# Kernel optimization log

Measured on AMD Instinct MI355X. Metric: run time of the kernel, lower is better.

The kernel has to match this reference:

```python
import jax, jax.numpy as jnp
from jax import lax
import numpy as np

SHAPE = (50, 60, 65)   # -> after net: (17, 27, 32), flatten = 14688
NEG = 0.01             # LeakyReLU default slope
B, N = 8, 80000        # batch size, total active voxels


def _lrelu(x):
    return jnp.where(x >= 0, x, NEG * x)


def _sparse_conv(x, w, b, m):
    # Regular (non-submanifold) sparse conv == dense VALID conv on densified
    # input (inactive sites are 0 so they contribute nothing). Output site is
    # active iff any input site in the kernel footprint is active; bias is
    # added only at active output sites.
    k = w.shape[2]
    y = lax.conv_general_dilated(x, w, (1, 1, 1), 'VALID',
                                 dimension_numbers=('NCDHW', 'OIDHW', 'NCDHW'))
    m2 = lax.reduce_window(m, 0.0, lax.max, (1, 1, k, k, k), (1, 1, 1, 1, 1), 'VALID')
    y = jnp.where(m2 > 0, y + b[None, :, None, None, None], 0.0)
    return y, m2


def _sparse_maxpool(x, m, k):
    # spconv SparseMaxPool: max over ACTIVE sites only (inactive excluded, not 0)
    xm = jnp.where(m > 0, x, -jnp.inf)
    p = lax.reduce_window(xm, -jnp.inf, lax.max, (1, 1, k, k, k), (1, 1, 1, 1, 1), 'VALID')
    m2 = lax.reduce_window(m, 0.0, lax.max, (1, 1, k, k, k), (1, 1, 1, 1, 1), 'VALID')
    return jnp.where(m2 > 0, p, 0.0), m2


def setup_inputs() -> dict:
    key = jax.random.key(0)
    ks = jax.random.split(key, 24)
    D, H, W = SHAPE
    features = jax.random.normal(ks[0], (N, 1), dtype=jnp.float32)
    bi = jax.random.randint(ks[1], (N,), 0, B)
    zi = jax.random.randint(ks[2], (N,), 0, D)
    yi = jax.random.randint(ks[3], (N,), 0, H)
    xi = jax.random.randint(ks[4], (N,), 0, W)
    coors = jnp.stack([bi, zi, yi, xi], axis=1).astype(jnp.int32)
    s = 0.05
    p = {}
    p['w1'] = jax.random.normal(ks[5], (32, 1, 4, 4, 4), jnp.float32) * s
    p['b1'] = jax.random.normal(ks[6], (32,), jnp.float32) * s
    p['w2'] = jax.random.normal(ks[7], (32, 32, 4, 4, 4), jnp.float32) * s
    p['b2'] = jax.random.normal(ks[8], (32,), jnp.float32) * s
    p['w3'] = jax.random.normal(ks[9], (32, 32, 4, 4, 4), jnp.float32) * s
    p['b3'] = jax.random.normal(ks[10], (32,), jnp.float32) * s
    p['w4'] = jax.random.normal(ks[11], (32, 32, 4, 4, 4), jnp.float32) * s
    p['b4'] = jax.random.normal(ks[12], (32,), jnp.float32) * s
    p['w5'] = jax.random.normal(ks[13], (32, 32, 4, 4, 4), jnp.float32) * s
    p['b5'] = jax.random.normal(ks[14], (32,), jnp.float32) * s
    p['w6'] = jax.random.normal(ks[15], (32, 32, 4, 4, 4), jnp.float32) * s
    p['b6'] = jax.random.normal(ks[16], (32,), jnp.float32) * s
    p['w7'] = jax.random.normal(ks[17], (1, 32, 4, 4, 4), jnp.float32) * s
    p['b7'] = jax.random.normal(ks[18], (1,), jnp.float32) * s
    p['W8'] = jax.random.normal(ks[19], (14688, 1000), jnp.float32) * 0.01
    p['b8'] = jax.random.normal(ks[20], (1000,), jnp.float32) * s
    p['W9'] = jax.random.normal(ks[21], (1000, 1000), jnp.float32) * 0.03
    p['b9'] = jax.random.normal(ks[22], (1000,), jnp.float32) * s
    p['W10'] = jax.random.normal(ks[23], (1000, 1), jnp.float32) * 0.03
    p['b10'] = jnp.zeros((1,), jnp.float32)
    return dict(features=features, coors=coors, batch_size=B, **p)


def reference(features, coors, batch_size,
              w1, b1, w2, b2, w3, b3, w4, b4, w5, b5, w6, b6, w7, b7,
              W8, b8, W9, b9, W10, b10):
    D, H, W = SHAPE
    bi, zi, yi, xi = coors[:, 0], coors[:, 1], coors[:, 2], coors[:, 3]
    dense = jnp.zeros((batch_size, 1, D, H, W), features.dtype)
    dense = dense.at[bi, 0, zi, yi, xi].set(features[:, 0])
    mask = jnp.zeros((batch_size, 1, D, H, W), features.dtype)
    mask = mask.at[bi, 0, zi, yi, xi].set(1.0)

    x, m = _sparse_conv(dense, w1, b1, mask); x = _lrelu(x)
    x, m = _sparse_conv(x, w2, b2, m);        x = _lrelu(x)
    x, m = _sparse_maxpool(x, m, 5)
    x, m = _sparse_conv(x, w3, b3, m);        x = _lrelu(x)
    x, m = _sparse_conv(x, w4, b4, m);        x = _lrelu(x)
    x, m = _sparse_maxpool(x, m, 5)
    x, m = _sparse_conv(x, w5, b5, m);        x = _lrelu(x)
    x, m = _sparse_conv(x, w6, b6, m);        x = _lrelu(x)
    x, m = _sparse_conv(x, w7, b7, m);        x = _lrelu(x)
    x, m = _sparse_maxpool(x, m, 5)

    # ToDense (inactive sites already 0) + Flatten -> [B, 14688]
    h = x.reshape(x.shape[0], -1)
    h = _lrelu(h @ W8 + b8)
    h = _lrelu(h @ W9 + b9)
    out = _lrelu(h @ W10 + b10)
    return out
```

## Files before the change

kernel.cpp:

```cpp
#include <hip/hip_runtime.h>
#include <cstddef>


#define NEGSLOPE 0.01f
#define NINF (-3.0e38f)

#define TZ 4
#define TY 4
#define TXT 16
#define IZ 7
#define IY 7
#define IX 19
#define NV (IZ*IY*IX)

typedef __attribute__((ext_vector_type(8)))  short    short8;
typedef __attribute__((ext_vector_type(4)))  unsigned uint4v;
typedef __attribute__((ext_vector_type(16))) float    floatx16;

__device__ __forceinline__ float lrelu(float v) { return v >= 0.f ? v : NEGSLOPE * v; }

__device__ __forceinline__ unsigned short f2bf(float f) {
  unsigned b = __float_as_uint(f);
  return (unsigned short)((b + 0x7fffu + ((b >> 16) & 1u)) >> 16);
}
__device__ __forceinline__ float bf2f(unsigned short h) {
  return __uint_as_float(((unsigned)h) << 16);
}
__device__ __forceinline__ unsigned splitpair(float a, float b, unsigned& lo) {
  unsigned short ha = f2bf(a), hb = f2bf(b);
  unsigned short la = f2bf(a - bf2f(ha)), lb = f2bf(b - bf2f(hb));
  lo = (unsigned)la | ((unsigned)lb << 16);
  return (unsigned)ha | ((unsigned)hb << 16);
}

__device__ __forceinline__ short8 ld_frag(const uint2* s2, int v, int oct) {
  uint2 u0 = s2[v * 5 + oct * 2];
  uint2 u1 = s2[v * 5 + oct * 2 + 1];
  uint4v t; t.x = u0.x; t.y = u0.y; t.z = u1.x; t.w = u1.y;
  return __builtin_bit_cast(short8, t);
}

__global__ void k_claim(const int* __restrict__ coors, unsigned* __restrict__ claim, int N) {
  int i = blockIdx.x * blockDim.x + threadIdx.x;
  if (i >= N) return;
  int b = coors[4*i], z = coors[4*i+1], y = coors[4*i+2], x = coors[4*i+3];
  int v = ((b*50 + z)*60 + y)*65 + x;
  atomicMax(&claim[v], (unsigned)(i + 1));
}

__global__ void k_scatter(const int* __restrict__ coors, const float* __restrict__ feat,
                          const unsigned* __restrict__ claim,
                          float* __restrict__ x0, float* __restrict__ m0, int N) {
  int i = blockIdx.x * blockDim.x + threadIdx.x;
  if (i >= N) return;
  int b = coors[4*i], z = coors[4*i+1], y = coors[4*i+2], x = coors[4*i+3];
  int v = ((b*50 + z)*60 + y)*65 + x;
  m0[v] = 1.f;
  if (claim[v] == (unsigned)(i + 1)) x0[v] = feat[i];
}

__global__ void k_repack(const float* __restrict__ w, float* __restrict__ wr, int CI, int CO) {
  int i = blockIdx.x * blockDim.x + threadIdx.x;
  int tot = CO * CI * 64;
  if (i >= tot) return;
  int k = i & 63;
  int ci = (i >> 6) % CI;
  int co = i / (64 * CI);
  wr[(k * CI + ci) * CO + co] = w[i];
}

__global__ void k_repack_mfma(const float* __restrict__ w, unsigned short* __restrict__ tbl) {
  int i = blockIdx.x * blockDim.x + threadIdx.x;
  if (i >= 64*4*2*64) return;
  int lane = i & 63; int t = i >> 6;
  int pack = t & 1; t >>= 1;
  int pass = t & 3; int tap = t >> 2;
  int co = lane & 31; int oct = lane >> 5;
#pragma unroll
  for (int j = 0; j < 8; ++j) {
    int k = oct * 8 + j;
    int ci = pass * 8 + (k & 7);
    int part = ((k >> 3) ^ pack) & 1;
    float wv = w[((co * 32 + ci) << 6) + tap];
    unsigned short wh = f2bf(wv);
    unsigned short r = part ? f2bf(wv - bf2f(wh)) : wh;
    tbl[(size_t)i * 8 + j] = r;
  }
}

__global__ void kd_z(const float* __restrict__ in, float* __restrict__ o,
                     int Zi, int Yi, int Xi, int Zo, int K, int nI) {
  int gid = blockIdx.x * blockDim.x + threadIdx.x;
  int perOut = Zo * Yi * Xi;
  if (gid >= nI * perOut) return;
  int item = gid / perOut;
  int r = gid - item * perOut;
  int x = r % Xi; int t = r / Xi;
  int y = t % Yi; int z = t / Yi;
  const float* ib = in + (size_t)item * Zi * Yi * Xi;
  float mx = 0.f;
  for (int d = 0; d < K; d++) mx = fmaxf(mx, ib[((z + d) * Yi + y) * Xi + x]);
  o[gid] = mx;
}

__global__ void kd_y(const float* __restrict__ in, float* __restrict__ o,
                     int Zo, int Yi, int Xi, int Yo, int K, int nI) {
  int gid = blockIdx.x * blockDim.x + threadIdx.x;
  int perOut = Zo * Yo * Xi;
  if (gid >= nI * perOut) return;
  int item = gid / perOut;
  int r = gid - item * perOut;
  int x = r % Xi; int t = r / Xi;
  int y = t % Yo; int z = t / Yo;
  const float* ib = in + (size_t)item * Zo * Yi * Xi;
  float mx = 0.f;
  for (int d = 0; d < K; d++) mx = fmaxf(mx, ib[(z * Yi + y + d) * Xi + x]);
  o[gid] = mx;
}

__global__ void kd_x(const float* __restrict__ in, float* __restrict__ o,
                     int Zo, int Yo, int Xi, int Xo, int K, int nI) {
  int gid = blockIdx.x * blockDim.x + threadIdx.x;
  int perOut = Zo * Yo * Xo;
  if (gid >= nI * perOut) return;
  int item = gid / perOut;
  int r = gid - item * perOut;
  int x = r % Xo; int t = r / Xo;
  int y = t % Yo; int z = t / Yo;
  const float* ib = in + (size_t)item * Zo * Yo * Xi;
  float mx = 0.f;
  for (int d = 0; d < K; d++) mx = fmaxf(mx, ib[(z * Yo + y) * Xi + x + d]);
  o[gid] = mx;
}

__global__ __launch_bounds__(256, 4)
void k_conv32m(const float* __restrict__ in, const unsigned short* __restrict__ tbl,
               const float* __restrict__ bias, const float* __restrict__ mo,
               float* __restrict__ out,
               int Zi, int Yi, int Xi, int Zo, int Yo, int Xo,
               int tilesZ, int tilesY, int tilesX) {
  __shared__ unsigned sU[NV * 10];
  const int perIn = Zi * Yi * Xi;
  const int perOut = Zo * Yo * Xo;
  int bid = blockIdx.x;
  int txi = bid % tilesX; bid /= tilesX;
  int tyi = bid % tilesY; bid /= tilesY;
  int tzi = bid % tilesZ; int item = bid / tilesZ;
  const int z0 = tzi * TZ, y0 = tyi * TY, x0 = txi * TXT;
  const int tid = threadIdx.x;
  const int lane = tid & 63;
  const int col = lane & 31;
  const int oct = lane >> 5;
  const int wv  = tid >> 6;

  int lvBase0, lvBase1;
  {
    int vt0 = (2*wv + 0)*32 + col;
    int vt1 = (2*wv + 1)*32 + col;
    lvBase0 = ((vt0 >> 6)*IY + ((vt0 >> 4) & 3))*IX + (vt0 & 15);
    lvBase1 = ((vt1 >> 6)*IY + ((vt1 >> 4) & 3))*IX + (vt1 & 15);
  }

  floatx16 acc0, acc1;
#pragma unroll
  for (int r = 0; r < 16; ++r) { acc0[r] = 0.f; acc1[r] = 0.f; }

  const float* inb = in + (size_t)item * perIn * 32;
  const char* tb = (const char*)tbl + lane * 16;
  uint2* s2 = (uint2*)sU;

#pragma unroll 1
  for (int p = 0; p < 4; ++p) {
    __syncthreads();
    for (int idx = tid; idx < NV; idx += 256) {
      int iz = idx / (IY * IX); int r = idx - iz * (IY * IX);
      int iy = r / IX; int ix = r - iy * IX;
      int gz = z0 + iz, gy = y0 + iy, gx = x0 + ix;
      float4 f0 = make_float4(0.f,0.f,0.f,0.f), f1 = make_float4(0.f,0.f,0.f,0.f);
      if (gz < Zi && gy < Yi && gx < Xi) {
        const float* vp = inb + (size_t)((gz * Yi + gy) * Xi + gx) * 32 + p * 8;
        f0 = *(const float4*)vp;
        f1 = *(const float4*)(vp + 4);
      }
      unsigned l0, l1, l2, l3;
      unsigned h0 = splitpair(f0.x, f0.y, l0);
      unsigned h1 = splitpair(f0.z, f0.w, l1);
      unsigned h2 = splitpair(f1.x, f1.y, l2);
      unsigned h3 = splitpair(f1.z, f1.w, l3);
      s2[idx * 5 + 0] = make_uint2(h0, h1);
      s2[idx * 5 + 1] = make_uint2(h2, h3);
      s2[idx * 5 + 2] = make_uint2(l0, l1);
      s2[idx * 5 + 3] = make_uint2(l2, l3);
    }
    __syncthreads();

    const char* tp = tb + (size_t)p * 2048;
#pragma unroll 2
    for (int tap = 0; tap < 64; ++tap) {
      int kz = tap >> 4, ky = (tap >> 2) & 3, kx = tap & 3;
      int sOff = (kz * IY + ky) * IX + kx;
      short8 b0 = *(const short8*)(tp + (size_t)tap * 8192);
      short8 b1 = *(const short8*)(tp + (size_t)tap * 8192 + 1024);
      short8 a0 = ld_frag(s2, lvBase0 + sOff, oct);
      short8 a1 = ld_frag(s2, lvBase1 + sOff, oct);
      acc0 = __builtin_amdgcn_mfma_f32_32x32x16_bf16(a0, b0, acc0, 0, 0, 0);
      acc0 = __builtin_amdgcn_mfma_f32_32x32x16_bf16(a0, b1, acc0, 0, 0, 0);
      acc1 = __builtin_amdgcn_mfma_f32_32x32x16_bf16(a1, b0, acc1, 0, 0, 0);
      acc1 = __builtin_amdgcn_mfma_f32_32x32x16_bf16(a1, b1, acc1, 0, 0, 0);
    }
  }

  const float bco = bias[col];
#pragma unroll
  for (int gg = 0; gg < 2; ++gg) {
    int vtb = (2*wv + gg) * 32;
#pragma unroll
    for (int rg = 0; rg < 16; ++rg) {
      int row = (rg & 3) + 8 * (rg >> 2) + 4 * oct;
      int vt = vtb + row;
      int oz = vt >> 6, oy = (vt >> 4) & 3, ox = vt & 15;
      int gz = z0 + oz, gy = y0 + oy, gx = x0 + ox;
      if (gz < Zo && gy < Yo && gx < Xo) {
        int ov = item * perOut + (gz * Yo + gy) * Xo + gx;
        float val = (gg == 0) ? acc0[rg] : acc1[rg];
        bool act = mo[ov] > 0.f;
        out[(size_t)ov * 32 + col] = lrelu(act ? (val + bco) : 0.f);
      }
    }
  }
}

__global__ __launch_bounds__(256, 2)
void k_conv1t(const float* __restrict__ in, const float* __restrict__ wr,
              const float* __restrict__ bias, const float* __restrict__ mo,
              float* __restrict__ out,
              int Zi, int Yi, int Xi, int Zo, int Yo, int Xo,
              int tilesZ, int tilesY, int tilesX) {
  __shared__ float sinf[NV];
  __shared__ float4 wsh[512];
  {
    const float4* wr4 = (const float4*)wr;
    for (int idx = threadIdx.x; idx < 512; idx += 256) wsh[idx] = wr4[idx];
  }
  const int perIn = Zi * Yi * Xi;
  const int perOut = Zo * Yo * Xo;
  int bid = blockIdx.x;
  int txi = bid % tilesX; bid /= tilesX;
  int tyi = bid % tilesY; bid /= tilesY;
  int tzi = bid % tilesZ; int item = bid / tilesZ;
  const int z0 = tzi * TZ, y0 = tyi * TY, x0 = txi * TXT;
  const int tid = threadIdx.x;
  const int ox = tid & 15, oy = (tid >> 4) & 3, oz = tid >> 6;

  const float* inb = in + (size_t)item * perIn;
  for (int idx = tid; idx < NV; idx += 256) {
    int iz = idx / (IY * IX); int r = idx - iz * (IY * IX);
    int iy = r / IX; int ix = r - iy * IX;
    int gz = z0 + iz, gy = y0 + iy, gx = x0 + ix;
    float val = 0.f;
    if (gz < Zi && gy < Yi && gx < Xi)
      val = inb[(size_t)((gz * Yi + gy) * Xi + gx)];
    sinf[idx] = val;
  }
  __syncthreads();

  float4 acc[8];
#pragma unroll
  for (int j = 0; j < 8; ++j) acc[j] = make_float4(0.f, 0.f, 0.f, 0.f);

#pragma unroll 1
  for (int tap = 0; tap < 64; ++tap) {
    int kz = tap >> 4, ky = (tap >> 2) & 3, kx = tap & 3;
    int lv = ((oz + kz) * IY + (oy + ky)) * IX + (ox + kx);
    float av = sinf[lv];
#pragma unroll
    for (int j = 0; j < 8; ++j) {
      float4 wvv = wsh[tap * 8 + j];
      acc[j].x = fmaf(av, wvv.x, acc[j].x);
      acc[j].y = fmaf(av, wvv.y, acc[j].y);
      acc[j].z = fmaf(av, wvv.z, acc[j].z);
      acc[j].w = fmaf(av, wvv.w, acc[j].w);
    }
  }

  int gz = z0 + oz, gy = y0 + oy, gx = x0 + ox;
  if (gz < Zo && gy < Yo && gx < Xo) {
    int ov = item * perOut + (gz * Yo + gy) * Xo + gx;
    bool act = mo[ov] > 0.f;
    const float4* b4 = (const float4*)bias;
    float* op = out + (size_t)ov * 32;
#pragma unroll
    for (int j = 0; j < 8; ++j) {
      float4 r = acc[j]; float4 bj = b4[j];
      r.x = lrelu(act ? (r.x + bj.x) : 0.f);
      r.y = lrelu(act ? (r.y + bj.y) : 0.f);
      r.z = lrelu(act ? (r.z + bj.z) : 0.f);
      r.w = lrelu(act ? (r.w + bj.w) : 0.f);
      *(float4*)(op + j * 4) = r;
    }
  }
}

__global__ __launch_bounds__(256, 2)
void k_conv7t(const float* __restrict__ in, const float* __restrict__ wr,
              const float* __restrict__ bias, const float* __restrict__ mo,
              float* __restrict__ out,
              int Zi, int Yi, int Xi, int Zo, int Yo, int Xo,
              int tilesZ, int tilesY, int tilesX) {
  __shared__ float4 sin4[4][NV];
  __shared__ float4 wsh[512];
  {
    const float4* wr4 = (const float4*)wr;
    for (int idx = threadIdx.x; idx < 512; idx += 256) wsh[idx] = wr4[idx];
  }
  const int perIn = Zi * Yi * Xi;
  const int perOut = Zo * Yo * Xo;
  int bid = blockIdx.x;
  int txi = bid % tilesX; bid /= tilesX;
  int tyi = bid % tilesY; bid /= tilesY;
  int tzi = bid % tilesZ; int item = bid / tilesZ;
  const int z0 = tzi * TZ, y0 = tyi * TY, x0 = txi * TXT;
  const int tid = threadIdx.x;
  const int ox = tid & 15, oy = (tid >> 4) & 3, oz = tid >> 6;

  const float* inb = in + (size_t)item * perIn * 32;
  float acc = 0.f;

#pragma unroll 1
  for (int h = 0; h < 2; ++h) {
    __syncthreads();
    for (int idx = tid; idx < NV * 4; idx += 256) {
      int q = idx / NV; int v = idx - q * NV;
      int iz = v / (IY * IX); int r = v - iz * (IY * IX);
      int iy = r / IX; int ix = r - iy * IX;
      int gz = z0 + iz, gy = y0 + iy, gx = x0 + ix;
      float4 val = make_float4(0.f, 0.f, 0.f, 0.f);
      if (gz < Zi && gy < Yi && gx < Xi)
        val = *(const float4*)(inb + (size_t)((gz * Yi + gy) * Xi + gx) * 32 + h * 16 + q * 4);
      sin4[q][v] = val;
    }
    __syncthreads();
#pragma unroll 1
    for (int tap = 0; tap < 64; ++tap) {
      int kz = tap >> 4, ky = (tap >> 2) & 3, kx = tap & 3;
      int lv = ((oz + kz) * IY + (oy + ky)) * IX + (ox + kx);
      float4 a0 = sin4[0][lv];
      float4 a1 = sin4[1][lv];
      float4 a2 = sin4[2][lv];
      float4 a3 = sin4[3][lv];
      float4 w0 = wsh[tap * 8 + h * 4 + 0];
      float4 w1 = wsh[tap * 8 + h * 4 + 1];
      float4 w2 = wsh[tap * 8 + h * 4 + 2];
      float4 w3 = wsh[tap * 8 + h * 4 + 3];
      acc += a0.x*w0.x + a0.y*w0.y + a0.z*w0.z + a0.w*w0.w
           + a1.x*w1.x + a1.y*w1.y + a1.z*w1.z + a1.w*w1.w
           + a2.x*w2.x + a2.y*w2.y + a2.z*w2.z + a2.w*w2.w
           + a3.x*w3.x + a3.y*w3.y + a3.z*w3.z + a3.w*w3.w;
    }
  }

  int gz = z0 + oz, gy = y0 + oy, gx = x0 + ox;
  if (gz < Zo && gy < Yo && gx < Xo) {
    int ov = item * perOut + (gz * Yo + gy) * Xo + gx;
    bool act = mo[ov] > 0.f;
    out[ov] = lrelu(act ? (acc + bias[0]) : 0.f);
  }
}

__global__ void k_pool_z(const float* __restrict__ in, const float* __restrict__ m,
                         float* __restrict__ out, int Zi, int Yi, int Xi, int Zo, int nI) {
  int gid = blockIdx.x * blockDim.x + threadIdx.x;
  int perOut = Zo * Yi * Xi;
  int tot = nI * perOut * 8;
  if (gid >= tot) return;
  int c4 = gid & 7; int v = gid >> 3;
  int item = v / perOut;
  int r = v - item * perOut;
  int x = r % Xi; int t = r / Xi;
  int y = t % Yi; int z = t / Yi;
  int ib = item * Zi * Yi * Xi;
  float4 acc = {NINF, NINF, NINF, NINF};
  for (int j = 0; j < 5; j++) {
    int vi = ib + ((z + j)*Yi + y)*Xi + x;
    if (m[vi] > 0.f) {
      float4 val = *(const float4*)(in + (size_t)vi*32 + c4*4);
      acc.x = fmaxf(acc.x, val.x); acc.y = fmaxf(acc.y, val.y);
      acc.z = fmaxf(acc.z, val.z); acc.w = fmaxf(acc.w, val.w);
    }
  }
  *(float4*)(out + (size_t)v*32 + c4*4) = acc;
}

__global__ void k_pool_y(const float* __restrict__ in, float* __restrict__ out,
                         int Z, int Yi, int Xi, int Yo, int nI) {
  int gid = blockIdx.x * blockDim.x + threadIdx.x;
  int perOut = Z * Yo * Xi;
  int tot = nI * perOut * 8;
  if (gid >= tot) return;
  int c4 = gid & 7; int v = gid >> 3;
  int item = v / perOut;
  int r = v - item * perOut;
  int x = r % Xi; int t = r / Xi;
  int y = t % Yo; int z = t / Yo;
  int ib = item * Z * Yi * Xi;
  float4 acc = {NINF, NINF, NINF, NINF};
  for (int j = 0; j < 5; j++) {
    int vi = ib + (z*Yi + y + j)*Xi + x;
    float4 val = *(const float4*)(in + (size_t)vi*32 + c4*4);
    acc.x = fmaxf(acc.x, val.x); acc.y = fmaxf(acc.y, val.y);
    acc.z = fmaxf(acc.z, val.z); acc.w = fmaxf(acc.w, val.w);
  }
  *(float4*)(out + (size_t)v*32 + c4*4) = acc;
}

__global__ void k_pool_x(const float* __restrict__ in, const float* __restrict__ mp,
                         float* __restrict__ out, int Z, int Y, int Xi, int Xo, int nI) {
  int gid = blockIdx.x * blockDim.x + threadIdx.x;
  int perOut = Z * Y * Xo;
  int tot = nI * perOut * 8;
  if (gid >= tot) return;
  int c4 = gid & 7; int v = gid >> 3;
  int item = v / perOut;
  int r = v - item * perOut;
  int x = r % Xo; int t = r / Xo;
  int y = t % Y; int z = t / Y;
  int ib = item * Z * Y * Xi;
  float4 acc = {NINF, NINF, NINF, NINF};
  for (int j = 0; j < 5; j++) {
    int vi = ib + (z*Y + y)*Xi + x + j;
    float4 val = *(const float4*)(in + (size_t)vi*32 + c4*4);
    acc.x = fmaxf(acc.x, val.x); acc.y = fmaxf(acc.y, val.y);
    acc.z = fmaxf(acc.z, val.z); acc.w = fmaxf(acc.w, val.w);
  }
  bool act = mp[v] > 0.f;
  float4 rr;
  rr.x = act ? acc.x : 0.f; rr.y = act ? acc.y : 0.f;
  rr.z = act ? acc.z : 0.f; rr.w = act ? acc.w : 0.f;
  *(float4*)(out + (size_t)v*32 + c4*4) = rr;
}

__global__ void k_pool3(const float* __restrict__ xin, const float* __restrict__ m,
                        const float* __restrict__ mp, float* __restrict__ out, int nI) {
  int gid = blockIdx.x * blockDim.x + threadIdx.x;
  int perOut = 17 * 27 * 32;
  int tot = nI * perOut;
  if (gid >= tot) return;
  int item = gid / perOut;
  int r = gid - item * perOut;
  int x = r & 31; int t = r >> 5;
  int y = t % 27; int z = t / 27;
  const float* xb = xin + (size_t)item * 23436;
  const float* mb = m + (size_t)item * 23436;
  float acc = NINF;
  for (int dz = 0; dz < 5; dz++)
    for (int dy = 0; dy < 5; dy++) {
      const float* rowx = xb + (size_t)(((z + dz)*31 + y + dy)*36 + x);
      const float* rowm = mb + (size_t)(((z + dz)*31 + y + dy)*36 + x);
      for (int dx = 0; dx < 5; dx++)
        if (rowm[dx] > 0.f) acc = fmaxf(acc, rowx[dx]);
    }
  out[gid] = (mp[gid] > 0.f) ? acc : 0.f;
}

__global__ __launch_bounds__(256, 4)
void k_fc_part(const float* __restrict__ X, const float* __restrict__ Wm,
               float* __restrict__ part, int K, int Ncol, int Kc) {
  __shared__ float sm[16][16][8];
  int ks = blockIdx.y;
  int k0 = ks * Kc;
  int k1 = k0 + Kc; if (k1 > K) k1 = K;
  int cl = threadIdx.x & 15;
  int kt = threadIdx.x >> 4;
  int col = blockIdx.x * 16 + cl;
  float a0=0.f,a1=0.f,a2=0.f,a3=0.f,a4=0.f,a5=0.f,a6=0.f,a7=0.f;
  if (col < Ncol) {
    for (int k = k0 + kt; k < k1; k += 16) {
      float w = Wm[(size_t)k * Ncol + col];
      a0 += X[0 * K + k] * w; a1 += X[1 * K + k] * w;
      a2 += X[2 * K + k] * w; a3 += X[3 * K + k] * w;
      a4 += X[4 * K + k] * w; a5 += X[5 * K + k] * w;
      a6 += X[6 * K + k] * w; a7 += X[7 * K + k] * w;
    }
  }
  sm[kt][cl][0]=a0; sm[kt][cl][1]=a1; sm[kt][cl][2]=a2; sm[kt][cl][3]=a3;
  sm[kt][cl][4]=a4; sm[kt][cl][5]=a5; sm[kt][cl][6]=a6; sm[kt][cl][7]=a7;
  __syncthreads();
  if (threadIdx.x < 128) {
    int c = threadIdx.x & 15;
    int b = threadIdx.x >> 4;
    float s = 0.f;
#pragma unroll
    for (int k = 0; k < 16; k++) s += sm[k][c][b];
    int cc = blockIdx.x * 16 + c;
    if (cc < Ncol) part[((size_t)ks * 8 + b) * Ncol + cc] = s;
  }
}

__global__ void k_fc_fin(const float* __restrict__ part, int ns,
                         const float* __restrict__ bias, float* __restrict__ out, int Ncol) {
  int i = blockIdx.x * blockDim.x + threadIdx.x;
  if (i >= 8 * Ncol) return;
  int b = i / Ncol;
  int c = i - b * Ncol;
  float s = 0.f;
  for (int ks = 0; ks < ns; ks++) s += part[((size_t)ks * 8 + b) * Ncol + c];
  out[i] = lrelu(s + bias[c]);
}

__global__ __launch_bounds__(256, 4)
void k_fc(const float* __restrict__ X, const float* __restrict__ Wm,
          const float* __restrict__ bias, float* __restrict__ out,
          int K, int Ncol) {
  __shared__ float sm[16][16][8];
  int cl = threadIdx.x & 15;
  int kt = threadIdx.x >> 4;
  int col = blockIdx.x * 16 + cl;
  float a0=0.f,a1=0.f,a2=0.f,a3=0.f,a4=0.f,a5=0.f,a6=0.f,a7=0.f;
  if (col < Ncol) {
    for (int k = kt; k < K; k += 16) {
      float w = Wm[(size_t)k * Ncol + col];
      a0 += X[0 * K + k] * w; a1 += X[1 * K + k] * w;
      a2 += X[2 * K + k] * w; a3 += X[3 * K + k] * w;
      a4 += X[4 * K + k] * w; a5 += X[5 * K + k] * w;
      a6 += X[6 * K + k] * w; a7 += X[7 * K + k] * w;
    }
  }
  sm[kt][cl][0]=a0; sm[kt][cl][1]=a1; sm[kt][cl][2]=a2; sm[kt][cl][3]=a3;
  sm[kt][cl][4]=a4; sm[kt][cl][5]=a5; sm[kt][cl][6]=a6; sm[kt][cl][7]=a7;
  __syncthreads();
  if (threadIdx.x < 128) {
    int c = threadIdx.x & 15;
    int b = threadIdx.x >> 4;
    float s = 0.f;
#pragma unroll
    for (int k = 0; k < 16; k++) s += sm[k][c][b];
    int cc = blockIdx.x * 16 + c;
    if (cc < Ncol) out[b * Ncol + cc] = lrelu(s + bias[cc]);
  }
}

static inline int G256(long long n) { return (int)((n + 255) / 256); }

extern "C" void kernel_launch(void* const* d_in, const int* in_sizes, int n_in,
                              void* d_out, int out_size, void* d_ws, size_t ws_size,
                              hipStream_t stream) {
  const float* feat  = (const float*)d_in[0];
  const int*   coors = (const int*)d_in[1];
  const float* w1 = (const float*)d_in[3];  const float* b1 = (const float*)d_in[4];
  const float* w2 = (const float*)d_in[5];  const float* b2 = (const float*)d_in[6];
  const float* w3 = (const float*)d_in[7];  const float* b3 = (const float*)d_in[8];
  const float* w4 = (const float*)d_in[9];  const float* b4 = (const float*)d_in[10];
  const float* w5 = (const float*)d_in[11]; const float* b5 = (const float*)d_in[12];
  const float* w6 = (const float*)d_in[13]; const float* b6 = (const float*)d_in[14];
  const float* w7 = (const float*)d_in[15]; const float* b7 = (const float*)d_in[16];
  const float* W8 = (const float*)d_in[17]; const float* b8 = (const float*)d_in[18];
  const float* W9 = (const float*)d_in[19]; const float* b9 = (const float*)d_in[20];
  const float* W10= (const float*)d_in[21]; const float* b10= (const float*)d_in[22];
  float* out = (float*)d_out;

  char* ws = (char*)d_ws;
  size_t off = 0;
  auto alloc = [&](size_t nfloats) -> float* {
    float* p = (float*)(ws + off);
    off += ((nfloats * 4 + 1023) / 1024) * 1024;
    return p;
  };

  float* x0  = alloc(1560000);
  float* m0  = alloc(1560000);
  float* m1  = alloc(8 * 166098);
  float* m2  = alloc(8 * 140184);
  float* mp1 = alloc(8 * 110000);
  float* m3  = alloc(8 * 90428);
  float* m4  = alloc(8 * 73304);
  float* mp2 = alloc(8 * 54000);
  float* m5  = alloc(8 * 41958);
  float* m6  = alloc(8 * 31824);
  float* m7  = alloc(8 * 23436);
  float* mp3 = alloc(8 * 14688);
  float* p3  = alloc(8 * 14688);
  float* dt1 = alloc(8 * 183300);
  float* dt2 = alloc(8 * 174135);
  float* wr1 = alloc(2048);
  float* wr7 = alloc(2048);
  unsigned short* tb2 = (unsigned short*)alloc(131072);
  unsigned short* tb3 = (unsigned short*)alloc(131072);
  unsigned short* tb4 = (unsigned short*)alloc(131072);
  unsigned short* tb5 = (unsigned short*)alloc(131072);
  unsigned short* tb6 = (unsigned short*)alloc(131072);
  float* part= alloc(64000);
  float* h8  = alloc(8000);
  float* h9  = alloc(8000);
  size_t fixedOff = off;

  const size_t perItemAB = ((size_t)5315136*4 + 1023)/1024*1024
                         + ((size_t)4485888*4 + 1023)/1024*1024
                         + ((size_t)23436*4 + 1023)/1024*1024;
  int G = 0;
  for (int g : {8, 4, 2, 1})
    if (fixedOff + (size_t)g * perItemAB <= ws_size) { G = g; break; }
  if (G == 0) return;

  float* A  = alloc((size_t)G * 5315136);
  float* Bb = alloc((size_t)G * 4485888);
  float* x7 = alloc((size_t)G * 23436);
  unsigned* claim = (unsigned*)A;

  hipMemsetAsync(claim, 0, 1560000 * 4, stream);
  hipMemsetAsync(x0,    0, 1560000 * 4, stream);
  hipMemsetAsync(m0,    0, 1560000 * 4, stream);

  k_repack<<<G256(32*1*64),  256, 0, stream>>>(w1, wr1, 1, 32);
  k_repack<<<G256(1*32*64),  256, 0, stream>>>(w7, wr7, 32, 1);
  k_repack_mfma<<<128, 256, 0, stream>>>(w2, tb2);
  k_repack_mfma<<<128, 256, 0, stream>>>(w3, tb3);
  k_repack_mfma<<<128, 256, 0, stream>>>(w4, tb4);
  k_repack_mfma<<<128, 256, 0, stream>>>(w5, tb5);
  k_repack_mfma<<<128, 256, 0, stream>>>(w6, tb6);

  const int N = 80000;
  k_claim  <<<G256(N), 256, 0, stream>>>(coors, claim, N);
  k_scatter<<<G256(N), 256, 0, stream>>>(coors, feat, claim, x0, m0, N);

  auto dil3 = [&](const float* src, float* dst,
                  int Zi, int Yi, int Xi, int Zo, int Yo, int Xo, int K) {
    kd_z<<<G256((long long)8*Zo*Yi*Xi), 256, 0, stream>>>(src, dt1, Zi,Yi,Xi, Zo, K, 8);
    kd_y<<<G256((long long)8*Zo*Yo*Xi), 256, 0, stream>>>(dt1, dt2, Zo,Yi,Xi, Yo, K, 8);
    kd_x<<<G256((long long)8*Zo*Yo*Xo), 256, 0, stream>>>(dt2, dst, Zo,Yo,Xi, Xo, K, 8);
  };
  dil3(m0,  m1,  50,60,65, 47,57,62, 4);
  dil3(m1,  m2,  47,57,62, 44,54,59, 4);
  dil3(m2,  mp1, 44,54,59, 40,50,55, 5);
  dil3(mp1, m3,  40,50,55, 37,47,52, 4);
  dil3(m3,  m4,  37,47,52, 34,44,49, 4);
  dil3(m4,  mp2, 34,44,49, 30,40,45, 5);
  dil3(mp2, m5,  30,40,45, 27,37,42, 4);
  dil3(m5,  m6,  27,37,42, 24,34,39, 4);
  dil3(m6,  m7,  24,34,39, 21,31,36, 4);
  dil3(m7,  mp3, 21,31,36, 17,27,32, 5);

  auto conv32 = [&](const float* in, const unsigned short* tbl, const float* bias,
                    const float* mo, float* o,
                    int Zi, int Yi, int Xi, int Zo, int Yo, int Xo, int nI) {
    int tz = (Zo + TZ - 1) / TZ, ty = (Yo + TY - 1) / TY, tx = (Xo + TXT - 1) / TXT;
    k_conv32m<<<nI * tz * ty * tx, 256, 0, stream>>>(
        in, tbl, bias, mo, o, Zi, Yi, Xi, Zo, Yo, Xo, tz, ty, tx);
  };

  for (int g0 = 0; g0 < 8; g0 += G) {
    const float* x0g  = x0  + (size_t)g0 * 195000;
    const float* m1g  = m1  + (size_t)g0 * 166098;
    const float* m2g  = m2  + (size_t)g0 * 140184;
    const float* mp1g = mp1 + (size_t)g0 * 110000;
    const float* m3g  = m3  + (size_t)g0 * 90428;
    const float* m4g  = m4  + (size_t)g0 * 73304;
    const float* mp2g = mp2 + (size_t)g0 * 54000;
    const float* m5g  = m5  + (size_t)g0 * 41958;
    const float* m6g  = m6  + (size_t)g0 * 31824;
    const float* m7g  = m7  + (size_t)g0 * 23436;
    const float* mp3g = mp3 + (size_t)g0 * 14688;

    {
      int tz = (47 + TZ - 1) / TZ, ty = (57 + TY - 1) / TY, tx = (62 + TXT - 1) / TXT;
      k_conv1t<<<G * tz * ty * tx, 256, 0, stream>>>(
          x0g, wr1, b1, m1g, A, 50,60,65, 47,57,62, tz, ty, tx);
    }
    conv32(A, tb2, b2, m2g, Bb, 47,57,62, 44,54,59, G);
    k_pool_z<<<G256((long long)G*127440*8), 256, 0, stream>>>(Bb, m2g,  A,  44,54,59, 40, G);
    k_pool_y<<<G256((long long)G*118000*8), 256, 0, stream>>>(A,  Bb, 40,54,59, 50, G);
    k_pool_x<<<G256((long long)G*110000*8), 256, 0, stream>>>(Bb, mp1g, A,  40,50,59, 55, G);
    conv32(A, tb3, b3, m3g, Bb, 40,50,55, 37,47,52, G);
    conv32(Bb, tb4, b4, m4g, A, 37,47,52, 34,44,49, G);
    k_pool_z<<<G256((long long)G*64680*8), 256, 0, stream>>>(A,  m4g,  Bb, 34,44,49, 30, G);
    k_pool_y<<<G256((long long)G*58800*8), 256, 0, stream>>>(Bb, A,  30,44,49, 40, G);
    k_pool_x<<<G256((long long)G*54000*8), 256, 0, stream>>>(A,  mp2g, Bb, 30,40,49, 45, G);
    conv32(Bb, tb5, b5, m5g, A, 30,40,45, 27,37,42, G);
    conv32(A, tb6, b6, m6g, Bb, 27,37,42, 24,34,39, G);
    {
      int tz = (21 + TZ - 1) / TZ, ty = (31 + TY - 1) / TY, tx = (36 + TXT - 1) / TXT;
      k_conv7t<<<G * tz * ty * tx, 256, 0, stream>>>(
          Bb, wr7, b7, m7g, x7, 24,34,39, 21,31,36, tz, ty, tx);
    }
    k_pool3<<<G256((long long)G*14688), 256, 0, stream>>>(
        x7, m7g, mp3g, p3 + (size_t)g0 * 14688, G);
  }

  k_fc_part<<<dim3(63, 8), 256, 0, stream>>>(p3, W8, part, 14688, 1000, 1836);
  k_fc_fin <<<G256(8000), 256, 0, stream>>>(part, 8, b8, h8, 1000);
  k_fc_part<<<dim3(63, 4), 256, 0, stream>>>(h8, W9, part, 1000, 1000, 250);
  k_fc_fin <<<G256(8000), 256, 0, stream>>>(part, 4, b9, h9, 1000);
  k_fc<<<1, 256, 0, stream>>>(h9, W10, b10, out, 1000, 1);
}
```

Before: 3.349 ms.

## Store conv activations pre-split into bf16 hi/lo layout and prefetch next channel slab

Producers of conv32 inputs (conv1, pool_x, and conv3/conv5 via a new splitOut flag) now write activations as interleaved bf16 high/low pairs in 128-byte per-voxel blocks. The conv kernel copies these straight into shared memory without per-element splitting, and it prefetches the next channel group into registers while the current group's MFMAs run. This removes the repeated float-to-bf16 split work from the conv staging loop and hides global load latency, at the cost of extra registers for the prefetch buffers and a tighter coupling of data layout between kernels.

```diff
diff --git a/kernel.cpp b/kernel.cpp
--- a/kernel.cpp
+++ b/kernel.cpp
@@ -136,7 +136,7 @@
 __global__ __launch_bounds__(256, 4)
 void k_conv32m(const float* __restrict__ in, const unsigned short* __restrict__ tbl,
                const float* __restrict__ bias, const float* __restrict__ mo,
-               float* __restrict__ out,
+               float* __restrict__ out, int splitOut,
                int Zi, int Yi, int Xi, int Zo, int Yo, int Xo,
                int tilesZ, int tilesY, int tilesX) {
   __shared__ unsigned sU[NV * 10];
@@ -165,34 +165,61 @@
 #pragma unroll
   for (int r = 0; r < 16; ++r) { acc0[r] = 0.f; acc1[r] = 0.f; }
 
-  const float* inb = in + (size_t)item * perIn * 32;
+  const char* inB = (const char*)in + (size_t)item * perIn * 128;
   const char* tb = (const char*)tbl + lane * 16;
   uint2* s2 = (uint2*)sU;
+
+  const char* gptr[4];
+  int lidx[4];
+#pragma unroll
+  for (int it = 0; it < 4; ++it) {
+    int idx = tid + it * 256;
+    gptr[it] = nullptr; lidx[it] = -1;
+    if (idx < NV) {
+      int iz = idx / (IY * IX); int r = idx - iz * (IY * IX);
+      int iy = r / IX; int ix = r - iy * IX;
+      int gz = z0 + iz, gy = y0 + iy, gx = x0 + ix;
+      lidx[it] = idx * 5;
+      if (gz < Zi && gy < Yi && gx < Xi)
+        gptr[it] = inB + (size_t)((gz * Yi + gy) * Xi + gx) * 128;
+    }
+  }
+
+  uint4 hreg[4], lreg[4];
+  const uint4 zz = make_uint4(0u, 0u, 0u, 0u);
+#pragma unroll
+  for (int it = 0; it < 4; ++it) {
+    hreg[it] = zz; lreg[it] = zz;
+    if (gptr[it]) {
+      hreg[it] = *(const uint4*)(gptr[it]);
+      lreg[it] = *(const uint4*)(gptr[it] + 16);
+    }
+  }
 
 #pragma unroll 1
   for (int p = 0; p < 4; ++p) {
     __syncthreads();
-    for (int idx = tid; idx < NV; idx += 256) {
-      int iz = idx / (IY * IX); int r = idx - iz * (IY * IX);
-      int iy = r / IX; int ix = r - iy * IX;
-      int gz = z0 + iz, gy = y0 + iy, gx = x0 + ix;
-      float4 f0 = make_float4(0.f,0.f,0.f,0.f), f1 = make_float4(0.f,0.f,0.f,0.f);
-      if (gz < Zi && gy < Yi && gx < Xi) {
-        const float* vp = inb + (size_t)((gz * Yi + gy) * Xi + gx) * 32 + p * 8;
-        f0 = *(const float4*)vp;
-        f1 = *(const float4*)(vp + 4);
+#pragma unroll
+    for (int it = 0; it < 4; ++it) {
+      if (lidx[it] >= 0) {
+        s2[lidx[it] + 0] = make_uint2(hreg[it].x, hreg[it].y);
+        s2[lidx[it] + 1] = make_uint2(hreg[it].z, hreg[it].w);
+        s2[lidx[it] + 2] = make_uint2(lreg[it].x, lreg[it].y);
+        s2[lidx[it] + 3] = make_uint2(lreg[it].z, lreg[it].w);
       }
-      unsigned l0, l1, l2, l3;
-      unsigned h0 = splitpair(f0.x, f0.y, l0);
-      unsigned h1 = splitpair(f0.z, f0.w, l1);
-      unsigned h2 = splitpair(f1.x, f1.y, l2);
-      unsigned h3 = splitpair(f1.z, f1.w, l3);
-      s2[idx * 5 + 0] = make_uint2(h0, h1);
-      s2[idx * 5 + 1] = make_uint2(h2, h3);
-      s2[idx * 5 + 2] = make_uint2(l0, l1);
-      s2[idx * 5 + 3] = make_uint2(l2, l3);
     }
     __syncthreads();
+    if (p < 3) {
+      int po = (p + 1) * 32;
+#pragma unroll
+      for (int it = 0; it < 4; ++it) {
+        hreg[it] = zz; lreg[it] = zz;
+        if (gptr[it]) {
+          hreg[it] = *(const uint4*)(gptr[it] + po);
+          lreg[it] = *(const uint4*)(gptr[it] + po + 16);
+        }
+      }
+    }
 
     const char* tp = tb + (size_t)p * 2048;
 #pragma unroll 2
@@ -224,7 +251,16 @@
         int ov = item * perOut + (gz * Yo + gy) * Xo + gx;
         float val = (gg == 0) ? acc0[rg] : acc1[rg];
         bool act = mo[ov] > 0.f;
-        out[(size_t)ov * 32 + col] = lrelu(act ? (val + bco) : 0.f);
+        float vv = lrelu(act ? (val + bco) : 0.f);
+        if (!splitOut) {
+          out[(size_t)ov * 32 + col] = vv;
+        } else {
+          unsigned short hs = f2bf(vv);
+          unsigned short ls = f2bf(vv - bf2f(hs));
+          char* op = (char*)out + (size_t)ov * 128 + ((col >> 3) << 5) + ((col & 7) << 1);
+          *(unsigned short*)op = hs;
+          *(unsigned short*)(op + 16) = ls;
+        }
       }
     }
   }
@@ -288,15 +324,26 @@
     int ov = item * perOut + (gz * Yo + gy) * Xo + gx;
     bool act = mo[ov] > 0.f;
     const float4* b4 = (const float4*)bias;
-    float* op = out + (size_t)ov * 32;
-#pragma unroll
-    for (int j = 0; j < 8; ++j) {
-      float4 r = acc[j]; float4 bj = b4[j];
-      r.x = lrelu(act ? (r.x + bj.x) : 0.f);
-      r.y = lrelu(act ? (r.y + bj.y) : 0.f);
-      r.z = lrelu(act ? (r.z + bj.z) : 0.f);
-      r.w = lrelu(act ? (r.w + bj.w) : 0.f);
-      *(float4*)(op + j * 4) = r;
+    char* op = (char*)out + (size_t)ov * 128;
+#pragma unroll
+    for (int pp = 0; pp < 4; ++pp) {
+      float4 r0 = acc[pp * 2], r1 = acc[pp * 2 + 1];
+      float4 b0 = b4[pp * 2], b1 = b4[pp * 2 + 1];
+      float v0 = lrelu(act ? (r0.x + b0.x) : 0.f);
+      float v1 = lrelu(act ? (r0.y + b0.y) : 0.f);
+      float v2 = lrelu(act ? (r0.z + b0.z) : 0.f);
+      float v3 = lrelu(act ? (r0.w + b0.w) : 0.f);
+      float v4 = lrelu(act ? (r1.x + b1.x) : 0.f);
+      float v5 = lrelu(act ? (r1.y + b1.y) : 0.f);
+      float v6 = lrelu(act ? (r1.z + b1.z) : 0.f);
+      float v7 = lrelu(act ? (r1.w + b1.w) : 0.f);
+      unsigned L0, L1, L2, L3;
+      unsigned H0 = splitpair(v0, v1, L0);
+      unsigned H1 = splitpair(v2, v3, L1);
+      unsigned H2 = splitpair(v4, v5, L2);
+      unsigned H3 = splitpair(v6, v7, L3);
+      *(uint4*)(op + pp * 32)      = make_uint4(H0, H1, H2, H3);
+      *(uint4*)(op + pp * 32 + 16) = make_uint4(L0, L1, L2, L3);
     }
   }
 }
@@ -436,7 +483,12 @@
   float4 rr;
   rr.x = act ? acc.x : 0.f; rr.y = act ? acc.y : 0.f;
   rr.z = act ? acc.z : 0.f; rr.w = act ? acc.w : 0.f;
-  *(float4*)(out + (size_t)v*32 + c4*4) = rr;
+  unsigned lo01, lo23;
+  unsigned h01 = splitpair(rr.x, rr.y, lo01);
+  unsigned h23 = splitpair(rr.z, rr.w, lo23);
+  char* op = (char*)out + (size_t)v * 128 + ((c4 >> 1) << 5) + ((c4 & 1) << 3);
+  *(uint2*)op        = make_uint2(h01, h23);
+  *(uint2*)(op + 16) = make_uint2(lo01, lo23);
 }
 
 __global__ void k_pool3(const float* __restrict__ xin, const float* __restrict__ m,
@@ -640,11 +692,11 @@
   dil3(m7,  mp3, 21,31,36, 17,27,32, 5);
 
   auto conv32 = [&](const float* in, const unsigned short* tbl, const float* bias,
-                    const float* mo, float* o,
+                    const float* mo, float* o, int splitOut,
                     int Zi, int Yi, int Xi, int Zo, int Yo, int Xo, int nI) {
     int tz = (Zo + TZ - 1) / TZ, ty = (Yo + TY - 1) / TY, tx = (Xo + TXT - 1) / TXT;
     k_conv32m<<<nI * tz * ty * tx, 256, 0, stream>>>(
-        in, tbl, bias, mo, o, Zi, Yi, Xi, Zo, Yo, Xo, tz, ty, tx);
+        in, tbl, bias, mo, o, splitOut, Zi, Yi, Xi, Zo, Yo, Xo, tz, ty, tx);
   };
 
   for (int g0 = 0; g0 < 8; g0 += G) {
@@ -665,17 +717,17 @@
       k_conv1t<<<G * tz * ty * tx, 256, 0, stream>>>(
           x0g, wr1, b1, m1g, A, 50,60,65, 47,57,62, tz, ty, tx);
     }
-    conv32(A, tb2, b2, m2g, Bb, 47,57,62, 44,54,59, G);
+    conv32(A, tb2, b2, m2g, Bb, 0, 47,57,62, 44,54,59, G);
     k_pool_z<<<G256((long long)G*127440*8), 256, 0, stream>>>(Bb, m2g,  A,  44,54,59, 40, G);
     k_pool_y<<<G256((long long)G*118000*8), 256, 0, stream>>>(A,  Bb, 40,54,59, 50, G);
     k_pool_x<<<G256((long long)G*110000*8), 256, 0, stream>>>(Bb, mp1g, A,  40,50,59, 55, G);
-    conv32(A, tb3, b3, m3g, Bb, 40,50,55, 37,47,52, G);
-    conv32(Bb, tb4, b4, m4g, A, 37,47,52, 34,44,49, G);
+    conv32(A, tb3, b3, m3g, Bb, 1, 40,50,55, 37,47,52, G);
+    conv32(Bb, tb4, b4, m4g, A, 0, 37,47,52, 34,44,49, G);
     k_pool_z<<<G256((long long)G*64680*8), 256, 0, stream>>>(A,  m4g,  Bb, 34,44,49, 30, G);
     k_pool_y<<<G256((long long)G*58800*8), 256, 0, stream>>>(Bb, A,  30,44,49, 40, G);
     k_pool_x<<<G256((long long)G*54000*8), 256, 0, stream>>>(A,  mp2g, Bb, 30,40,49, 45, G);
-    conv32(Bb, tb5, b5, m5g, A, 30,40,45, 27,37,42, G);
-    conv32(A, tb6, b6, m6g, Bb, 27,37,42, 24,34,39, G);
+    conv32(Bb, tb5, b5, m5g, A, 1, 30,40,45, 27,37,42, G);
+    conv32(A, tb6, b6, m6g, Bb, 0, 27,37,42, 24,34,39, G);
     {
       int tz = (21 + TZ - 1) / TZ, ty = (31 + TY - 1) / TY, tx = (36 + TXT - 1) / TXT;
       k_conv7t<<<G * tz * ty * tx, 256, 0, stream>>>(
```

Measured after the change: 3.431 ms. +2.4%, slower.
